# Performance work log

Hardware: AMD Instinct MI355X
Metric: run time of the kernel (lower is better)

The kernel has to match this reference:

```python
import jax, jax.numpy as jnp
import numpy as np
import math

M_BITS = 256


def setup_inputs() -> dict:
    key = jax.random.key(0)
    k1, k2, k3, k4, k5, k6 = jax.random.split(key, 6)
    B, N, D, MB, DH = 8, 2048, 1024, M_BITS, 128
    return {
        "Q": jax.random.normal(k1, (B, N, D), dtype=jnp.float32),
        "K": jax.random.normal(k2, (B, N, D), dtype=jnp.float32),
        "V": jax.random.normal(k3, (B, N, D), dtype=jnp.float32),
        "Wq": jax.random.normal(k4, (D, MB), dtype=jnp.float32) / math.sqrt(D),
        "Wk": jax.random.normal(k5, (D, MB), dtype=jnp.float32) / math.sqrt(D),
        "Wv": jax.random.normal(k6, (D, DH), dtype=jnp.float32) / math.sqrt(D),
    }


def reference(Q, K, V, Wq, Wk, Wv):
    # Boolean REWA encoding: project then hard-binarize (sign bits).
    # sim(q,k) = #matching bits = (s_q . s_k + m) / 2 with s = 2*bit - 1.
    m = Wq.shape[1]
    scale = 1.0 / math.sqrt(m)
    sq = jnp.where(jnp.einsum('bnd,dm->bnm', Q, Wq) > 0, 1.0, -1.0)  # [B,N,m]
    sk = jnp.where(jnp.einsum('bkd,dm->bkm', K, Wk) > 0, 1.0, -1.0)  # [B,M,m]
    dot = jnp.einsum('bnm,bkm->bnk', sq, sk)                         # [B,N,M]
    scores = 0.5 * (dot + m) * scale
    attn = jax.nn.softmax(scores, axis=-1)                           # [B,N,M]
    Vp = jnp.einsum('bkd,dh->bkh', V, Wv)                            # [B,M,d_head]
    out = jnp.einsum('bnk,bkh->bnh', attn, Vp)                       # [B,N,d_head]
    return out, attn
```

## Files before the change

kernel.cpp:

```cpp
#include <hip/hip_runtime.h>


typedef __attribute__((ext_vector_type(4))) float f32x4;
typedef __attribute__((ext_vector_type(8))) __bf16 bf16x8;

#define FLAG_CAP 32768
#define FLAG_TAU 2e-4f

__device__ inline unsigned short f2b(float x) {
    unsigned int u = __float_as_uint(x);
    return (unsigned short)((u + 0x7FFFu + ((u >> 16) & 1u)) >> 16);
}

__global__ __launch_bounds__(256) void prep_weights(
    const float* __restrict__ Wq, const float* __restrict__ Wk, const float* __restrict__ Wv,
    unsigned short* __restrict__ WqhT, unsigned short* __restrict__ WqlT,
    unsigned short* __restrict__ WkhT, unsigned short* __restrict__ WklT,
    unsigned short* __restrict__ WvhT, int* __restrict__ flag_count)
{
    if (blockIdx.x == 0 && threadIdx.x == 0) *flag_count = 0;
    int i = blockIdx.x * 256 + threadIdx.x;
    const float* src; unsigned short *dh, *dl; int cols, j;
    if (i < 262144)      { src = Wq; dh = WqhT; dl = WqlT; cols = 256; j = i; }
    else if (i < 524288) { src = Wk; dh = WkhT; dl = WklT; cols = 256; j = i - 262144; }
    else                 { src = Wv; dh = WvhT; dl = nullptr; cols = 128; j = i - 524288; }
    int d = j / cols, m = j % cols;
    float x = src[j];
    unsigned short h = f2b(x);
    dh[(size_t)m * 1024 + d] = h;
    if (dl) {
        float hf = __uint_as_float(((unsigned int)h) << 16);
        dl[(size_t)m * 1024 + d] = f2b(x - hf);
    }
}

__global__ __launch_bounds__(256) void proj_kernel(
    const float* __restrict__ Q, const float* __restrict__ K, const float* __restrict__ V,
    const unsigned short* __restrict__ WqhT, const unsigned short* __restrict__ WqlT,
    const unsigned short* __restrict__ WkhT, const unsigned short* __restrict__ WklT,
    const unsigned short* __restrict__ WvhT,
    unsigned short* __restrict__ Sq, unsigned short* __restrict__ Sk,
    unsigned short* __restrict__ VpT,
    int* __restrict__ flag_count, int* __restrict__ flags)
{
    const int z = blockIdx.z, y = blockIdx.y;
    if (z == 2 && y == 1) return;
    const int m0 = blockIdx.x * 64;
    const bool split = (z < 2);
    const int n0 = split ? y * 128 : 0;
    const float* src = (z == 0) ? Q : (z == 1) ? K : V;
    const unsigned short* BhT = (z == 0) ? WqhT : (z == 1) ? WkhT : WvhT;
    const unsigned short* BlT = (z == 0) ? WqlT : WklT;

    __shared__ __align__(16) unsigned short smem[15360];
    unsigned short* Ah = smem;
    unsigned short* Al = smem + 2560;
    unsigned short* Bh = smem + 5120;
    unsigned short* Bl = smem + 10240;

    const int tid = threadIdx.x;
    const int wid = tid >> 6, lane = tid & 63;
    const int lr = lane & 15, lg = lane >> 4;

    const int arow = tid >> 2, aquad = tid & 3;
    const float* abase = src + (size_t)(m0 + arow) * 1024 + aquad * 8;
    const int brow = tid >> 1, bhalf = tid & 1;
    const unsigned short* bhbase = BhT + (size_t)(n0 + brow) * 1024 + bhalf * 16;
    const unsigned short* blbase = BlT + (size_t)(n0 + brow) * 1024 + bhalf * 16;

    float4 av0, av1;
    uint4 bh0, bh1, bl0, bl1;

    auto load_tile = [&](int k0) {
        av0 = *(const float4*)(abase + k0);
        av1 = *(const float4*)(abase + k0 + 4);
        bh0 = *(const uint4*)(bhbase + k0);
        bh1 = *(const uint4*)(bhbase + k0 + 8);
        if (split) {
            bl0 = *(const uint4*)(blbase + k0);
            bl1 = *(const uint4*)(blbase + k0 + 8);
        }
    };
    auto write_tile = [&]() {
        float xs[8] = {av0.x, av0.y, av0.z, av0.w, av1.x, av1.y, av1.z, av1.w};
        __bf16 hs[8], ls[8];
        #pragma unroll
        for (int i = 0; i < 8; ++i) {
            __bf16 h = (__bf16)xs[i];
            hs[i] = h;
            ls[i] = (__bf16)(xs[i] - (float)h);
        }
        *(uint4*)(Ah + arow * 40 + aquad * 8) = *(const uint4*)hs;
        if (split) *(uint4*)(Al + arow * 40 + aquad * 8) = *(const uint4*)ls;
        *(uint4*)(Bh + brow * 40 + bhalf * 16) = bh0;
        *(uint4*)(Bh + brow * 40 + bhalf * 16 + 8) = bh1;
        if (split) {
            *(uint4*)(Bl + brow * 40 + bhalf * 16) = bl0;
            *(uint4*)(Bl + brow * 40 + bhalf * 16 + 8) = bl1;
        }
    };

    f32x4 acc[8];
    #pragma unroll
    for (int t = 0; t < 8; ++t) acc[t] = f32x4{0.f, 0.f, 0.f, 0.f};

    load_tile(0);
    write_tile();
    __syncthreads();

    for (int ks = 0; ks < 32; ++ks) {
        if (ks < 31) load_tile((ks + 1) * 32);
        const bf16x8 a_h = *(const bf16x8*)(Ah + (wid * 16 + lr) * 40 + lg * 8);
        bf16x8 a_l;
        if (split) a_l = *(const bf16x8*)(Al + (wid * 16 + lr) * 40 + lg * 8);
        #pragma unroll
        for (int t = 0; t < 8; ++t) {
            const bf16x8 b_h = *(const bf16x8*)(Bh + (t * 16 + lr) * 40 + lg * 8);
            acc[t] = __builtin_amdgcn_mfma_f32_16x16x32_bf16(a_h, b_h, acc[t], 0, 0, 0);
            if (split) {
                const bf16x8 b_l = *(const bf16x8*)(Bl + (t * 16 + lr) * 40 + lg * 8);
                acc[t] = __builtin_amdgcn_mfma_f32_16x16x32_bf16(a_h, b_l, acc[t], 0, 0, 0);
                acc[t] = __builtin_amdgcn_mfma_f32_16x16x32_bf16(a_l, b_h, acc[t], 0, 0, 0);
            }
        }
        if (ks < 31) {
            __syncthreads();
            write_tile();
            __syncthreads();
        }
    }

    if (z < 2) {
        unsigned short* dst = (z == 0) ? Sq : Sk;
        const int whichbit = z << 22;
        #pragma unroll
        for (int t = 0; t < 8; ++t)
            #pragma unroll
            for (int j = 0; j < 4; ++j) {
                const int row = m0 + wid * 16 + 4 * lg + j;
                const int col = n0 + t * 16 + lr;
                const float zv = acc[t][j];
                dst[(size_t)row * 256 + col] =
                    (zv > 0.f) ? (unsigned short)0x3F80 : (unsigned short)0xBF80;
                if (__builtin_fabsf(zv) < FLAG_TAU) {
                    int slot = atomicAdd(flag_count, 1);
                    if (slot < FLAG_CAP) flags[slot] = whichbit | (row << 8) | col;
                }
            }
    } else {
        __syncthreads();
        unsigned short* tp = smem;
        #pragma unroll
        for (int t = 0; t < 8; ++t)
            #pragma unroll
            for (int j = 0; j < 4; ++j) {
                const int h = t * 16 + lr;
                const int key = wid * 16 + 4 * lg + j;
                tp[h * 72 + key] = f2b(acc[t][j]);
            }
        __syncthreads();
        const int b = m0 >> 11, key0 = m0 & 2047;
        const int h = tid >> 1, half = tid & 1;
        const unsigned short* sp = tp + h * 72 + half * 32;
        unsigned short* gp = VpT + (size_t)(b * 128 + h) * 2048 + key0 + half * 32;
        #pragma unroll
        for (int i = 0; i < 4; ++i)
            *(uint4*)(gp + i * 8) = *(const uint4*)(sp + i * 8);
    }
}

__global__ __launch_bounds__(256) void fixup_kernel(
    const float* __restrict__ Q, const float* __restrict__ K,
    const float* __restrict__ Wq, const float* __restrict__ Wk,
    unsigned short* __restrict__ Sq, unsigned short* __restrict__ Sk,
    const int* __restrict__ flag_count, const int* __restrict__ flags)
{
    const int nflags = min(*flag_count, FLAG_CAP);
    const int wave = (int)(blockIdx.x * 256 + threadIdx.x) >> 6;
    const int lane = threadIdx.x & 63;
    const int nwaves = gridDim.x * 4;
    for (int i = wave; i < nflags; i += nwaves) {
        const int enc = flags[i];
        const int which = enc >> 22;
        const int row = (enc >> 8) & 0x3FFF;
        const int col = enc & 255;
        const float* srow = (which ? K : Q) + (size_t)row * 1024;
        const float* W = (which ? Wk : Wq) + col;
        double accd = 0.0;
        #pragma unroll 4
        for (int d = lane; d < 1024; d += 64)
            accd += (double)srow[d] * (double)W[(size_t)d * 256];
        #pragma unroll
        for (int off = 32; off; off >>= 1) accd += __shfl_xor(accd, off);
        if (lane == 0)
            (which ? Sk : Sq)[(size_t)row * 256 + col] =
                (accd > 0.0) ? (unsigned short)0x3F80 : (unsigned short)0xBF80;
    }
}

__global__ __launch_bounds__(256) void attn_kernel(
    const unsigned short* __restrict__ Sq, const unsigned short* __restrict__ Sk,
    const unsigned short* __restrict__ VpT,
    float* __restrict__ attn, float* __restrict__ out_or_part,
    float* __restrict__ rowsum_part, int nsplit)
{
    const int b = blockIdx.y;
    const int q0 = blockIdx.x * 64;
    const int sp = blockIdx.z;
    const int tid = threadIdx.x;
    const int wid = tid >> 6, lane = tid & 63;
    const int lr = lane & 15, lg = lane >> 4;

    __shared__ __align__(16) unsigned short sk_lds[32][264];
    __shared__ __align__(16) unsigned short vpt_lds[128][40];
    __shared__ __align__(16) unsigned short e_lds[4][16][40];

    uint4 sqf[8];
    {
        const unsigned short* p =
            Sq + (size_t)(b * 2048 + q0 + wid * 16 + lr) * 256 + lg * 8;
        #pragma unroll
        for (int s = 0; s < 8; ++s) sqf[s] = *(const uint4*)(p + s * 32);
    }

    f32x4 oacc[8];
    #pragma unroll
    for (int t = 0; t < 8; ++t) oacc[t] = f32x4{0.f, 0.f, 0.f, 0.f};
    float racc[4] = {0.f, 0.f, 0.f, 0.f};

    float* attn_row_base = attn + (size_t)(b * 2048 + q0 + wid * 16 + 4 * lg) * 2048;

    const int tiles = 64 / nsplit;
    for (int kt = sp * tiles; kt < sp * tiles + tiles; ++kt) {
        const int kt0 = kt * 32;
        __syncthreads();
        {
            const int row = tid >> 3, chunk = tid & 7;
            const unsigned short* p = Sk + (size_t)(b * 2048 + kt0 + row) * 256 + chunk * 32;
            uint4 v0 = *(const uint4*)(p);
            uint4 v1 = *(const uint4*)(p + 8);
            uint4 v2 = *(const uint4*)(p + 16);
            uint4 v3 = *(const uint4*)(p + 24);
            unsigned short* q = &sk_lds[row][chunk * 32];
            *(uint4*)(q) = v0; *(uint4*)(q + 8) = v1;
            *(uint4*)(q + 16) = v2; *(uint4*)(q + 24) = v3;
        }
        {
            const int h = tid >> 1, half = tid & 1;
            const unsigned short* p = VpT + (size_t)(b * 128 + h) * 2048 + kt0 + half * 16;
            uint4 v0 = *(const uint4*)(p);
            uint4 v1 = *(const uint4*)(p + 8);
            unsigned short* q = &vpt_lds[h][half * 16];
            *(uint4*)(q) = v0; *(uint4*)(q + 8) = v1;
        }
        __syncthreads();

        f32x4 dacc[2];
        dacc[0] = f32x4{0.f, 0.f, 0.f, 0.f};
        dacc[1] = f32x4{0.f, 0.f, 0.f, 0.f};
        #pragma unroll
        for (int s = 0; s < 8; ++s) {
            const bf16x8 a = *(const bf16x8*)(&sqf[s]);
            #pragma unroll
            for (int t2 = 0; t2 < 2; ++t2) {
                const bf16x8 bk = *(const bf16x8*)(&sk_lds[t2 * 16 + lr][s * 32 + lg * 8]);
                dacc[t2] = __builtin_amdgcn_mfma_f32_16x16x32_bf16(a, bk, dacc[t2], 0, 0, 0);
            }
        }
        #pragma unroll
        for (int t2 = 0; t2 < 2; ++t2)
            #pragma unroll
            for (int j = 0; j < 4; ++j) {
                float e = __expf((dacc[t2][j] + 256.0f) * 0.03125f);
                racc[j] += e;
                attn_row_base[(size_t)j * 2048 + kt0 + t2 * 16 + lr] = e;
                e_lds[wid][4 * lg + j][t2 * 16 + lr] = f2b(e);
            }
        const bf16x8 ea = *(const bf16x8*)(&e_lds[wid][lr][lg * 8]);
        #pragma unroll
        for (int t = 0; t < 8; ++t) {
            const bf16x8 vb = *(const bf16x8*)(&vpt_lds[t * 16 + lr][lg * 8]);
            oacc[t] = __builtin_amdgcn_mfma_f32_16x16x32_bf16(ea, vb, oacc[t], 0, 0, 0);
        }
    }

    #pragma unroll
    for (int j = 0; j < 4; ++j) {
        float v = racc[j];
        v += __shfl_xor(v, 1);
        v += __shfl_xor(v, 2);
        v += __shfl_xor(v, 4);
        v += __shfl_xor(v, 8);
        racc[j] = v;
    }
    if (lr == 0) {
        #pragma unroll
        for (int j = 0; j < 4; ++j)
            rowsum_part[sp * 16384 + b * 2048 + q0 + wid * 16 + 4 * lg + j] = racc[j];
    }
    if (nsplit == 1) {
        #pragma unroll
        for (int t = 0; t < 8; ++t)
            #pragma unroll
            for (int j = 0; j < 4; ++j)
                out_or_part[(size_t)(b * 2048 + q0 + wid * 16 + 4 * lg + j) * 128
                            + t * 16 + lr] = oacc[t][j] / racc[j];
    } else {
        #pragma unroll
        for (int t = 0; t < 8; ++t)
            #pragma unroll
            for (int j = 0; j < 4; ++j)
                out_or_part[((size_t)sp * 16384 + b * 2048 + q0 + wid * 16 + 4 * lg + j) * 128
                            + t * 16 + lr] = oacc[t][j];
    }
}

__global__ __launch_bounds__(256) void out_finalize(
    float* __restrict__ out, const float* __restrict__ out_part,
    const float* __restrict__ rowsum_part, int nsplit)
{
    const int idx4 = blockIdx.x * 256 + threadIdx.x;
    const int row = idx4 >> 5;
    float rs = 0.f;
    for (int k = 0; k < nsplit; ++k) rs += rowsum_part[k * 16384 + row];
    float4 s = {0.f, 0.f, 0.f, 0.f};
    const float4* p = (const float4*)out_part;
    for (int k = 0; k < nsplit; ++k) {
        float4 v = p[(size_t)k * 524288 + idx4];
        s.x += v.x; s.y += v.y; s.z += v.z; s.w += v.w;
    }
    const float inv = 1.0f / rs;
    float4 r = {s.x * inv, s.y * inv, s.z * inv, s.w * inv};
    ((float4*)out)[idx4] = r;
}

__global__ __launch_bounds__(256) void normalize_kernel(
    float* __restrict__ attn, const float* __restrict__ rowsum_part, int nsplit)
{
    const size_t idx4 = (size_t)blockIdx.x * 256 + threadIdx.x;
    const int row = (int)(idx4 >> 9);
    float rs = 0.f;
    for (int k = 0; k < nsplit; ++k) rs += rowsum_part[k * 16384 + row];
    const float inv = 1.0f / rs;
    float4* p = (float4*)attn + idx4;
    float4 v = *p;
    v.x *= inv; v.y *= inv; v.z *= inv; v.w *= inv;
    *p = v;
}

extern "C" void kernel_launch(void* const* d_in, const int* in_sizes, int n_in,
                              void* d_out, int out_size, void* d_ws, size_t ws_size,
                              hipStream_t stream)
{
    const float* Q  = (const float*)d_in[0];
    const float* K  = (const float*)d_in[1];
    const float* V  = (const float*)d_in[2];
    const float* Wq = (const float*)d_in[3];
    const float* Wk = (const float*)d_in[4];
    const float* Wv = (const float*)d_in[5];

    unsigned short* ws   = (unsigned short*)d_ws;
    unsigned short* WqhT = ws;
    unsigned short* WqlT = WqhT + 262144;
    unsigned short* WkhT = WqlT + 262144;
    unsigned short* WklT = WkhT + 262144;
    unsigned short* WvhT = WklT + 262144;
    unsigned short* Sq   = WvhT + 131072;
    unsigned short* Sk   = Sq + 4194304;
    unsigned short* VpT  = Sk + 4194304;
    int* flag_count    = (int*)(VpT + 2097152);
    int* flags         = flag_count + 1;
    float* rowsum_part = (float*)(flags + FLAG_CAP);
    const size_t fixed_bytes = (size_t)((char*)rowsum_part - (char*)d_ws);

    int nsplit = 1;
    if (ws_size >= fixed_bytes + 4u * (16384u + 2097152u) * sizeof(float)) nsplit = 4;
    else if (ws_size >= fixed_bytes + 2u * (16384u + 2097152u) * sizeof(float)) nsplit = 2;

    float* out_part = rowsum_part + (size_t)nsplit * 16384;

    float* out  = (float*)d_out;
    float* attn = out + 2097152;

    prep_weights<<<2560, 256, 0, stream>>>(Wq, Wk, Wv, WqhT, WqlT, WkhT, WklT, WvhT,
                                           flag_count);
    proj_kernel<<<dim3(256, 2, 3), 256, 0, stream>>>(Q, K, V, WqhT, WqlT, WkhT, WklT, WvhT,
                                                     Sq, Sk, VpT, flag_count, flags);
    fixup_kernel<<<64, 256, 0, stream>>>(Q, K, Wq, Wk, Sq, Sk, flag_count, flags);
    attn_kernel<<<dim3(32, 8, nsplit), 256, 0, stream>>>(
        Sq, Sk, VpT, attn, (nsplit == 1) ? out : out_part, rowsum_part, nsplit);
    if (nsplit > 1)
        out_finalize<<<2048, 256, 0, stream>>>(out, out_part, rowsum_part, nsplit);
    normalize_kernel<<<32768, 256, 0, stream>>>(attn, rowsum_part, nsplit);
}
```

Measured before the change: 482.5 us.

## Widen projection tile to full 256 columns so each A tile is loaded once

The projection kernel now computes all 256 output columns per block instead of splitting them across two blocks. Each Q/K row tile is therefore read from global memory and split into bf16 hi/lo only once rather than twice. In exchange each block does twice the MFMA work, uses more shared memory and twice the accumulators, and the grid shrinks to 768 blocks. A launch-bounds occupancy hint is added to cap register use.

After: 480.6 us. About the same (-0.4%).

```diff
diff --git a/kernel.cpp b/kernel.cpp
--- a/kernel.cpp
+++ b/kernel.cpp
@@ -34,7 +34,7 @@
     }
 }
 
-__global__ __launch_bounds__(256) void proj_kernel(
+__global__ __launch_bounds__(256, 3) void proj_kernel(
     const float* __restrict__ Q, const float* __restrict__ K, const float* __restrict__ V,
     const unsigned short* __restrict__ WqhT, const unsigned short* __restrict__ WqlT,
     const unsigned short* __restrict__ WkhT, const unsigned short* __restrict__ WklT,
@@ -43,20 +43,18 @@
     unsigned short* __restrict__ VpT,
     int* __restrict__ flag_count, int* __restrict__ flags)
 {
-    const int z = blockIdx.z, y = blockIdx.y;
-    if (z == 2 && y == 1) return;
+    const int z = blockIdx.y;
     const int m0 = blockIdx.x * 64;
     const bool split = (z < 2);
-    const int n0 = split ? y * 128 : 0;
     const float* src = (z == 0) ? Q : (z == 1) ? K : V;
     const unsigned short* BhT = (z == 0) ? WqhT : (z == 1) ? WkhT : WvhT;
     const unsigned short* BlT = (z == 0) ? WqlT : WklT;
 
-    __shared__ __align__(16) unsigned short smem[15360];
+    __shared__ __align__(16) unsigned short smem[25600];
     unsigned short* Ah = smem;
     unsigned short* Al = smem + 2560;
     unsigned short* Bh = smem + 5120;
-    unsigned short* Bl = smem + 10240;
+    unsigned short* Bl = smem + 15360;
 
     const int tid = threadIdx.x;
     const int wid = tid >> 6, lane = tid & 63;
@@ -64,21 +62,28 @@
 
     const int arow = tid >> 2, aquad = tid & 3;
     const float* abase = src + (size_t)(m0 + arow) * 1024 + aquad * 8;
-    const int brow = tid >> 1, bhalf = tid & 1;
-    const unsigned short* bhbase = BhT + (size_t)(n0 + brow) * 1024 + bhalf * 16;
-    const unsigned short* blbase = BlT + (size_t)(n0 + brow) * 1024 + bhalf * 16;
+    const int brow = tid;
+    const bool bvalid = split || (tid < 128);
+    const unsigned short* bhbase = BhT + (size_t)brow * 1024;
+    const unsigned short* blbase = BlT + (size_t)brow * 1024;
 
     float4 av0, av1;
-    uint4 bh0, bh1, bl0, bl1;
+    uint4 bh0, bh1, bh2, bh3, bl0, bl1, bl2, bl3;
 
     auto load_tile = [&](int k0) {
         av0 = *(const float4*)(abase + k0);
         av1 = *(const float4*)(abase + k0 + 4);
-        bh0 = *(const uint4*)(bhbase + k0);
-        bh1 = *(const uint4*)(bhbase + k0 + 8);
-        if (split) {
-            bl0 = *(const uint4*)(blbase + k0);
-            bl1 = *(const uint4*)(blbase + k0 + 8);
+        if (bvalid) {
+            bh0 = *(const uint4*)(bhbase + k0);
+            bh1 = *(const uint4*)(bhbase + k0 + 8);
+            bh2 = *(const uint4*)(bhbase + k0 + 16);
+            bh3 = *(const uint4*)(bhbase + k0 + 24);
+            if (split) {
+                bl0 = *(const uint4*)(blbase + k0);
+                bl1 = *(const uint4*)(blbase + k0 + 8);
+                bl2 = *(const uint4*)(blbase + k0 + 16);
+                bl3 = *(const uint4*)(blbase + k0 + 24);
+            }
         }
     };
     auto write_tile = [&]() {
@@ -92,17 +97,23 @@
         }
         *(uint4*)(Ah + arow * 40 + aquad * 8) = *(const uint4*)hs;
         if (split) *(uint4*)(Al + arow * 40 + aquad * 8) = *(const uint4*)ls;
-        *(uint4*)(Bh + brow * 40 + bhalf * 16) = bh0;
-        *(uint4*)(Bh + brow * 40 + bhalf * 16 + 8) = bh1;
-        if (split) {
-            *(uint4*)(Bl + brow * 40 + bhalf * 16) = bl0;
-            *(uint4*)(Bl + brow * 40 + bhalf * 16 + 8) = bl1;
+        if (bvalid) {
+            *(uint4*)(Bh + brow * 40)      = bh0;
+            *(uint4*)(Bh + brow * 40 + 8)  = bh1;
+            *(uint4*)(Bh + brow * 40 + 16) = bh2;
+            *(uint4*)(Bh + brow * 40 + 24) = bh3;
+            if (split) {
+                *(uint4*)(Bl + brow * 40)      = bl0;
+                *(uint4*)(Bl + brow * 40 + 8)  = bl1;
+                *(uint4*)(Bl + brow * 40 + 16) = bl2;
+                *(uint4*)(Bl + brow * 40 + 24) = bl3;
+            }
         }
     };
 
-    f32x4 acc[8];
+    f32x4 acc[16];
     #pragma unroll
-    for (int t = 0; t < 8; ++t) acc[t] = f32x4{0.f, 0.f, 0.f, 0.f};
+    for (int t = 0; t < 16; ++t) acc[t] = f32x4{0.f, 0.f, 0.f, 0.f};
 
     load_tile(0);
     write_tile();
@@ -111,16 +122,21 @@
     for (int ks = 0; ks < 32; ++ks) {
         if (ks < 31) load_tile((ks + 1) * 32);
         const bf16x8 a_h = *(const bf16x8*)(Ah + (wid * 16 + lr) * 40 + lg * 8);
-        bf16x8 a_l;
-        if (split) a_l = *(const bf16x8*)(Al + (wid * 16 + lr) * 40 + lg * 8);
-        #pragma unroll
-        for (int t = 0; t < 8; ++t) {
-            const bf16x8 b_h = *(const bf16x8*)(Bh + (t * 16 + lr) * 40 + lg * 8);
-            acc[t] = __builtin_amdgcn_mfma_f32_16x16x32_bf16(a_h, b_h, acc[t], 0, 0, 0);
-            if (split) {
+        if (split) {
+            const bf16x8 a_l = *(const bf16x8*)(Al + (wid * 16 + lr) * 40 + lg * 8);
+            #pragma unroll
+            for (int t = 0; t < 16; ++t) {
+                const bf16x8 b_h = *(const bf16x8*)(Bh + (t * 16 + lr) * 40 + lg * 8);
                 const bf16x8 b_l = *(const bf16x8*)(Bl + (t * 16 + lr) * 40 + lg * 8);
+                acc[t] = __builtin_amdgcn_mfma_f32_16x16x32_bf16(a_h, b_h, acc[t], 0, 0, 0);
                 acc[t] = __builtin_amdgcn_mfma_f32_16x16x32_bf16(a_h, b_l, acc[t], 0, 0, 0);
                 acc[t] = __builtin_amdgcn_mfma_f32_16x16x32_bf16(a_l, b_h, acc[t], 0, 0, 0);
+            }
+        } else {
+            #pragma unroll
+            for (int t = 0; t < 8; ++t) {
+                const bf16x8 b_h = *(const bf16x8*)(Bh + (t * 16 + lr) * 40 + lg * 8);
+                acc[t] = __builtin_amdgcn_mfma_f32_16x16x32_bf16(a_h, b_h, acc[t], 0, 0, 0);
             }
         }
         if (ks < 31) {
@@ -130,15 +146,15 @@
         }
     }
 
-    if (z < 2) {
+    if (split) {
         unsigned short* dst = (z == 0) ? Sq : Sk;
         const int whichbit = z << 22;
         #pragma unroll
-        for (int t = 0; t < 8; ++t)
+        for (int t = 0; t < 16; ++t)
             #pragma unroll
             for (int j = 0; j < 4; ++j) {
                 const int row = m0 + wid * 16 + 4 * lg + j;
-                const int col = n0 + t * 16 + lr;
+                const int col = t * 16 + lr;
                 const float zv = acc[t][j];
                 dst[(size_t)row * 256 + col] =
                     (zv > 0.f) ? (unsigned short)0x3F80 : (unsigned short)0xBF80;
@@ -384,8 +400,8 @@
 
     prep_weights<<<2560, 256, 0, stream>>>(Wq, Wk, Wv, WqhT, WqlT, WkhT, WklT, WvhT,
                                            flag_count);
-    proj_kernel<<<dim3(256, 2, 3), 256, 0, stream>>>(Q, K, V, WqhT, WqlT, WkhT, WklT, WvhT,
-                                                     Sq, Sk, VpT, flag_count, flags);
+    proj_kernel<<<dim3(256, 3), 256, 0, stream>>>(Q, K, V, WqhT, WqlT, WkhT, WklT, WvhT,
+                                                  Sq, Sk, VpT, flag_count, flags);
     fixup_kernel<<<64, 256, 0, stream>>>(Q, K, Wq, Wk, Sq, Sk, flag_count, flags);
     attn_kernel<<<dim3(32, 8, nsplit), 256, 0, stream>>>(
         Sq, Sk, VpT, attn, (nsplit == 1) ? out : out_part, rowsum_part, nsplit);
```
